# Performance work log

Measured on AMD Instinct MI355X. Metric: run time of the kernel, lower is better.

The kernel has to match this reference:

```python
import jax, jax.numpy as jnp
import numpy as np

N_NODES = 50000
N_EDGES = 800000
IN_DIM = 128
HIDDEN = 64
HEADS = 4
OUT_DIM = 64
NEG_SLOPE = 0.2


def setup_inputs() -> dict:
    key = jax.random.key(0)
    ks = jax.random.split(key, 16)
    def lin(k, fan_in, fan_out):
        return jax.random.normal(k, (fan_in, fan_out), dtype=jnp.float32) * (1.0 / np.sqrt(fan_in))
    def attn(k):
        return jax.random.normal(k, (HEADS, HIDDEN), dtype=jnp.float32) * 0.1
    inp = {
        "x": jax.random.normal(ks[0], (N_NODES, IN_DIM), dtype=jnp.float32),
        "src": jax.random.randint(ks[1], (N_EDGES,), 0, N_NODES, dtype=jnp.int32),
        "dst": jax.random.randint(ks[2], (N_EDGES,), 0, N_NODES, dtype=jnp.int32),
        # layer 0: in_dim -> heads*hidden
        "W0": lin(ks[3], IN_DIM, HEADS * HIDDEN),
        "al0": attn(ks[4]),
        "ar0": attn(ks[5]),
        # layer 1: heads*hidden -> heads*hidden
        "W1": lin(ks[6], HEADS * HIDDEN, HEADS * HIDDEN),
        "al1": attn(ks[7]),
        "ar1": attn(ks[8]),
        # final layer: heads*hidden -> heads*out_dim
        "W2": lin(ks[9], HEADS * HIDDEN, HEADS * OUT_DIM),
        "al2": jax.random.normal(ks[10], (HEADS, OUT_DIM), dtype=jnp.float32) * 0.1,
        "ar2": jax.random.normal(ks[11], (HEADS, OUT_DIM), dtype=jnp.float32) * 0.1,
        # output head: out_dim -> 1
        "Wout": lin(ks[12], OUT_DIM, 1),
        "bout": jnp.zeros((1,), dtype=jnp.float32),
    }
    return inp


def gat_layer(x, src, dst, W, al, ar):
    """DGL-style multi-head graph attention conv (edge gather/softmax/aggregate)."""
    N = x.shape[0]
    H, D = al.shape
    h = (x @ W).reshape(N, H, D)                      # [N,H,D]
    el = jnp.sum(h * al, axis=-1)                     # [N,H]
    er = jnp.sum(h * ar, axis=-1)                     # [N,H]
    e = jax.nn.leaky_relu(el[src] + er[dst], NEG_SLOPE)   # [E,H]
    # numerically-stable edge softmax segmented by destination node
    m = jax.ops.segment_max(e, dst, num_segments=N)   # [N,H]
    m = jnp.where(jnp.isfinite(m), m, 0.0)
    ex = jnp.exp(e - m[dst])                          # [E,H]
    denom = jax.ops.segment_sum(ex, dst, num_segments=N)  # [N,H]
    alpha = ex / (denom[dst] + 1e-9)                  # [E,H]
    msg = h[src] * alpha[..., None]                   # [E,H,D] (dominant traffic)
    out = jax.ops.segment_sum(msg, dst, num_segments=N)   # [N,H,D]
    return jax.nn.elu(out)


def reference(x, src, dst, W0, al0, ar0, W1, al1, ar1, W2, al2, ar2, Wout, bout):
    N = x.shape[0]
    # layer 0 (threshold layer also produces node index split index1/index0)
    h = gat_layer(x, src, dst, W0, al0, ar0)          # [N,H,HID]
    h = h.reshape(N, -1)                              # flatten(start=1,end=2)
    # middle layer
    h = gat_layer(h, src, dst, W1, al1, ar1)
    h = h.reshape(N, -1)
    # final layer + head-mean pool
    feats = gat_layer(h, src, dst, W2, al2, ar2)      # [N,H,OUT]
    feats = feats.mean(axis=1)                        # [N,OUT]
    out = jax.nn.relu(feats @ Wout + bout)            # [N,1]
    return out
```

## Files before the change

kernel.cpp:

```cpp
#include <hip/hip_runtime.h>
#include <hip/hip_fp16.h>
#include <math.h>

#define NN 50000
#define NE 800000
#define HEADS 4
#define HID 64
#define HD 256
#define NEG_SLOPE 0.2f
#define CSR_CAP 64

typedef __attribute__((ext_vector_type(8))) short short8;
typedef __attribute__((ext_vector_type(4))) float f32x4;
typedef __attribute__((ext_vector_type(2))) unsigned int uint2v;

__device__ __forceinline__ unsigned short f2bf(float f) {
    unsigned u = __float_as_uint(f);
    u += 0x7fff + ((u >> 16) & 1);
    return (unsigned short)(u >> 16);
}
__device__ __forceinline__ float bf2f(unsigned short b) {
    return __uint_as_float(((unsigned)b) << 16);
}

__device__ __forceinline__ float h2f_bits(unsigned short b) {
    __half_raw r; r.x = b;
    return __half2float(__half(r));
}
__device__ __forceinline__ unsigned short f2h_bits(float f) {
    __half_raw r(__float2half(f));
    return r.x;
}

__device__ __forceinline__ void wsplit_one(const float* W, unsigned short* Wf, int idx) {
    int lane = idx & 63;
    int tile = (idx >> 6) & 15;
    int kb   = idx >> 10;
    int col  = tile * 16 + (lane & 15);
    int krow = kb * 32 + (lane >> 4) * 8;
    unsigned short* p = Wf + ((size_t)(kb * 16 + tile) * 2 * 64 + lane) * 8;
#pragma unroll
    for (int j = 0; j < 8; j++) {
        float v = W[(size_t)(krow + j) * HD + col];
        unsigned short h = f2bf(v);
        unsigned short l = f2bf(v - bf2f(h));
        p[j] = h;
        p[512 + j] = l;
    }
}

__global__ __launch_bounds__(256) void prep_kernel(
    const float* __restrict__ W0, unsigned short* __restrict__ Wf0,
    const float* __restrict__ W1, unsigned short* __restrict__ Wf1,
    const float* __restrict__ W2, unsigned short* __restrict__ Wf2,
    int* __restrict__ cnt) {
    int b = (int)blockIdx.x;
    if (b < 80) {
        int idx = b * 256 + (int)threadIdx.x;
        const int n0 = 4 * 16 * 64;
        const int n1 = 8 * 16 * 64;
        if (idx < n0) wsplit_one(W0, Wf0, idx);
        else if (idx < n0 + n1) wsplit_one(W1, Wf1, idx - n0);
        else if (idx < n0 + 2 * n1) wsplit_one(W2, Wf2, idx - n0 - n1);
    } else {
        int base = (b - 80) * 1024 + (int)threadIdx.x;
#pragma unroll
        for (int j = 0; j < 4; j++) {
            int i = base + j * 256;
            if (i < NN) cnt[i] = 0;
        }
    }
}

__device__ __forceinline__ void gemm_epilogue(
    f32x4 (&acc)[4][4], int rowBase, int w, int mrow, int q,
    ushort* __restrict__ H, const float* __restrict__ al, const float* __restrict__ ar,
    float* __restrict__ el, float* __restrict__ er) {
    int n0 = w * 64;
    float alv[4], arv[4];
#pragma unroll
    for (int c = 0; c < 4; c++) {
        alv[c] = al[n0 + c * 16 + mrow];
        arv[c] = ar[n0 + c * 16 + mrow];
    }
#pragma unroll
    for (int r = 0; r < 4; r++) {
        float pl[4] = {0.f, 0.f, 0.f, 0.f};
        float pr[4] = {0.f, 0.f, 0.f, 0.f};
#pragma unroll
        for (int c = 0; c < 4; c++)
#pragma unroll
            for (int g = 0; g < 4; g++) {
                pl[g] += acc[r][c][g] * alv[c];
                pr[g] += acc[r][c][g] * arv[c];
            }
#pragma unroll
        for (int g = 0; g < 4; g++) {
#pragma unroll
            for (int off = 1; off < 16; off <<= 1) {
                pl[g] += __shfl_xor(pl[g], off);
                pr[g] += __shfl_xor(pr[g], off);
            }
        }
#pragma unroll
        for (int g = 0; g < 4; g++) {
            int row = rowBase + r * 16 + q * 4 + g;
            if (row < NN) {
#pragma unroll
                for (int c = 0; c < 4; c++)
                    H[(size_t)row * HD + n0 + c * 16 + mrow] = f2h_bits(acc[r][c][g]);
                if (mrow == 0) {
                    el[row * 4 + w] = pl[g];
                    er[row * 4 + w] = pr[g];
                }
            }
        }
    }
}

__device__ __forceinline__ void mfma_gemm_body_f32(
    int bid,
    const float* __restrict__ Xf,
    const unsigned short* __restrict__ Wf,
    ushort* __restrict__ H,
    const float* __restrict__ al, const float* __restrict__ ar,
    float* __restrict__ el, float* __restrict__ er,
    ushort* ldsA) {
    constexpr int K = 128;
    constexpr int KB = K / 32;
    int tid = (int)threadIdx.x;
    int w = tid >> 6;
    int lane = tid & 63;
    int rowBase = bid * 64;
    int mrow = lane & 15;
    int q = lane >> 4;

    f32x4 acc[4][4];
#pragma unroll
    for (int r = 0; r < 4; r++)
#pragma unroll
        for (int c = 0; c < 4; c++) {
            f32x4 z = {0.f, 0.f, 0.f, 0.f};
            acc[r][c] = z;
        }

    int srow = tid >> 2, qq = tid & 3;
    int grow = rowBase + srow;
    grow = grow < NN ? grow : NN - 1;
    int sr = srow >> 4, smrow = srow & 15;
    int flane = qq * 16 + smrow;
    ushort* sHi = &ldsA[((size_t)(sr * 2 + 0) * 64 + flane) * 8];

    float4 rf00, rf01, rf10, rf11;

    auto loadA0 = [&](int kb) {
        const float* xp = Xf + (size_t)grow * K + kb * 32 + qq * 8;
        rf00 = *(const float4*)xp;
        rf01 = *(const float4*)(xp + 4);
    };
    auto loadA1 = [&](int kb) {
        const float* xp = Xf + (size_t)grow * K + kb * 32 + qq * 8;
        rf10 = *(const float4*)xp;
        rf11 = *(const float4*)(xp + 4);
    };
    auto cvt8 = [&](float4 a, float4 b, short8& h8, short8& l8) {
        float vv[8] = {a.x, a.y, a.z, a.w, b.x, b.y, b.z, b.w};
#pragma unroll
        for (int j = 0; j < 8; j++) {
            unsigned short hh = f2bf(vv[j]);
            h8[j] = (short)hh;
            l8[j] = (short)f2bf(vv[j] - bf2f(hh));
        }
    };
    auto storeA0 = [&]() {
        short8 h8, l8;
        cvt8(rf00, rf01, h8, l8);
        *(short8*)sHi = h8;
        *(short8*)(sHi + 512) = l8;
    };
    auto storeA1 = [&]() {
        short8 h8, l8;
        cvt8(rf10, rf11, h8, l8);
        *(short8*)(sHi + 4096) = h8;
        *(short8*)(sHi + 4096 + 512) = l8;
    };

    auto compute = [&](int kb, int pofs) {
        short8 Wh[4], Wl_[4];
#pragma unroll
        for (int c = 0; c < 4; c++) {
            const unsigned short* wp =
                Wf + (((size_t)(kb * 16 + w * 4 + c) * 2) * 64 + lane) * 8;
            Wh[c]  = *(const short8*)wp;
            Wl_[c] = *(const short8*)(wp + 512);
        }
        short8 Ah[4], Al_[4];
#pragma unroll
        for (int r = 0; r < 4; r++) {
            Ah[r]  = *(const short8*)&ldsA[pofs + ((r * 2 + 0) * 64 + lane) * 8];
            Al_[r] = *(const short8*)&ldsA[pofs + ((r * 2 + 1) * 64 + lane) * 8];
        }
#pragma unroll
        for (int c = 0; c < 4; c++)
#pragma unroll
            for (int r = 0; r < 4; r++) {
                acc[r][c] = __builtin_amdgcn_mfma_f32_16x16x32_bf16(Ah[r],  Wh[c],  acc[r][c], 0, 0, 0);
                acc[r][c] = __builtin_amdgcn_mfma_f32_16x16x32_bf16(Ah[r],  Wl_[c], acc[r][c], 0, 0, 0);
                acc[r][c] = __builtin_amdgcn_mfma_f32_16x16x32_bf16(Al_[r], Wh[c],  acc[r][c], 0, 0, 0);
            }
    };

    loadA0(0);
    loadA1(1);
    for (int kb = 0; kb < KB; kb += 2) {
        __syncthreads();
        storeA0();
        storeA1();
        __syncthreads();
        if (kb + 2 < KB) {
            loadA0(kb + 2);
            loadA1(kb + 3);
        }
        compute(kb, 0);
        compute(kb + 1, 4096);
    }

    gemm_epilogue(acc, rowBase, w, mrow, q, H, al, ar, el, er);
}

__global__ __launch_bounds__(256, 3) void gemm0_scatter_kernel(
    const float* __restrict__ Xf, const unsigned short* __restrict__ Wf,
    ushort* __restrict__ H,
    const float* __restrict__ al, const float* __restrict__ ar,
    float* __restrict__ el, float* __restrict__ er,
    const int* __restrict__ src, const int* __restrict__ dst,
    int* __restrict__ cnt, int* __restrict__ csr_src) {
    __shared__ ushort ldsA[2 * 8 * 64 * 8];
    int b = (int)blockIdx.x;
    int g = b / 5, rem = b % 5;
    if (rem == 0) {
        mfma_gemm_body_f32(g, Xf, Wf, H, al, ar, el, er, ldsA);
    } else {
        int e = (g * 4 + (rem - 1)) * 256 + (int)threadIdx.x;
        if (e < NE) {
            int d = dst[e];
            int slot = atomicAdd(&cnt[d], 1);
            csr_src[(size_t)d * CSR_CAP + slot] = src[e];
        }
    }
}

__global__ __launch_bounds__(256, 2) void mfma_gemm_fullk_kernel(
    const ushort* __restrict__ Xh, const ushort* __restrict__ Xl,
    const unsigned short* __restrict__ Wf,
    ushort* __restrict__ H,
    const float* __restrict__ al, const float* __restrict__ ar,
    float* __restrict__ el, float* __restrict__ er) {
    constexpr int K = 256;
    constexpr int KB = K / 32;
    __shared__ ushort ldsA[KB * 4 * 2 * 64 * 8];
    int tid = (int)threadIdx.x;
    int w = tid >> 6;
    int lane = tid & 63;
    int rowBase = (int)blockIdx.x * 64;
    int mrow = lane & 15;
    int q = lane >> 4;

    int srow = tid >> 2, qq = tid & 3;
    int grow = rowBase + srow;
    grow = grow < NN ? grow : NN - 1;
    int sr = srow >> 4, smrow = srow & 15;
    int flane = qq * 16 + smrow;
    const ushort* xhp = Xh + (size_t)grow * K + qq * 8;
    const ushort* xlp = Xl + (size_t)grow * K + qq * 8;

    short8 sh[KB], sl[KB];
#pragma unroll
    for (int kb = 0; kb < KB; kb++) {
        sh[kb] = *(const short8*)(xhp + kb * 32);
        sl[kb] = *(const short8*)(xlp + kb * 32);
    }
#pragma unroll
    for (int kb = 0; kb < KB; kb++) {
        *(short8*)&ldsA[((size_t)(kb * 8 + sr * 2 + 0) * 64 + flane) * 8] = sh[kb];
        *(short8*)&ldsA[((size_t)(kb * 8 + sr * 2 + 1) * 64 + flane) * 8] = sl[kb];
    }
    __syncthreads();

    f32x4 acc[4][4];
#pragma unroll
    for (int r = 0; r < 4; r++)
#pragma unroll
        for (int c = 0; c < 4; c++) {
            f32x4 z = {0.f, 0.f, 0.f, 0.f};
            acc[r][c] = z;
        }

    for (int kb = 0; kb < KB; kb++) {
        const ushort* Abase = &ldsA[(size_t)kb * 8 * 512];
        short8 Wh[4], Wl_[4];
#pragma unroll
        for (int c = 0; c < 4; c++) {
            const unsigned short* wp =
                Wf + (((size_t)(kb * 16 + w * 4 + c) * 2) * 64 + lane) * 8;
            Wh[c]  = *(const short8*)wp;
            Wl_[c] = *(const short8*)(wp + 512);
        }
        short8 Ah[4], Al_[4];
#pragma unroll
        for (int r = 0; r < 4; r++) {
            Ah[r]  = *(const short8*)&Abase[((r * 2 + 0) * 64 + lane) * 8];
            Al_[r] = *(const short8*)&Abase[((r * 2 + 1) * 64 + lane) * 8];
        }
#pragma unroll
        for (int c = 0; c < 4; c++)
#pragma unroll
            for (int r = 0; r < 4; r++) {
                acc[r][c] = __builtin_amdgcn_mfma_f32_16x16x32_bf16(Ah[r],  Wh[c],  acc[r][c], 0, 0, 0);
                acc[r][c] = __builtin_amdgcn_mfma_f32_16x16x32_bf16(Ah[r],  Wl_[c], acc[r][c], 0, 0, 0);
                acc[r][c] = __builtin_amdgcn_mfma_f32_16x16x32_bf16(Al_[r], Wh[c],  acc[r][c], 0, 0, 0);
            }
    }

    gemm_epilogue(acc, rowBase, w, mrow, q, H, al, ar, el, er);
}

__device__ __forceinline__ float lrelu(float x) { return fmaxf(x, NEG_SLOPE * x); }

__device__ __forceinline__ float4 us4tof4(ushort4 u) {
    float4 f;
    f.x = h2f_bits(u.x); f.y = h2f_bits(u.y);
    f.z = h2f_bits(u.z); f.w = h2f_bits(u.w);
    return f;
}

template <int FINAL>
__global__ __launch_bounds__(256) void gat_node_kernel(
    const ushort* __restrict__ H, const float* __restrict__ el, const float* __restrict__ er,
    const int* __restrict__ cnt, const int* __restrict__ csr_src,
    ushort* __restrict__ out_hi, ushort* __restrict__ out_lo,
    const float* __restrict__ Wout, const float* __restrict__ bout,
    float* __restrict__ final_out) {
    int wave = threadIdx.x >> 6, lane = threadIdx.x & 63;
    int v = blockIdx.x * 4 + wave;
    if (v >= NN) return;
    int beg = v * CSR_CAP;
    int end = beg + cnt[v];

    int hh = lane >> 4;
    float er_h = er[v * 4 + hh];
    const float* elh = el + hh;
    unsigned lane4 = (unsigned)(lane * 4);

    float ss0 = 0.f, ss1 = 0.f, ss2 = 0.f, ss3 = 0.f;
    float4 a0 = make_float4(0.f, 0.f, 0.f, 0.f);
    float4 a1 = make_float4(0.f, 0.f, 0.f, 0.f);
    float4 a2 = make_float4(0.f, 0.f, 0.f, 0.f);
    float4 a3 = make_float4(0.f, 0.f, 0.f, 0.f);
    {
        int i = beg;
        for (; i + 4 <= end; i += 4) {
            unsigned s0 = (unsigned)csr_src[i];
            unsigned s1 = (unsigned)csr_src[i + 1];
            unsigned s2 = (unsigned)csr_src[i + 2];
            unsigned s3 = (unsigned)csr_src[i + 3];
            ushort4 q0 = *(const ushort4*)(H + ((s0 << 8) + lane4));
            ushort4 q1 = *(const ushort4*)(H + ((s1 << 8) + lane4));
            ushort4 q2 = *(const ushort4*)(H + ((s2 << 8) + lane4));
            ushort4 q3 = *(const ushort4*)(H + ((s3 << 8) + lane4));
            float w0 = __expf(lrelu(elh[s0 * 4u] + er_h));
            float w1 = __expf(lrelu(elh[s1 * 4u] + er_h));
            float w2 = __expf(lrelu(elh[s2 * 4u] + er_h));
            float w3 = __expf(lrelu(elh[s3 * 4u] + er_h));
            float4 h0 = us4tof4(q0);
            float4 h1 = us4tof4(q1);
            float4 h2 = us4tof4(q2);
            float4 h3 = us4tof4(q3);
            ss0 += w0; ss1 += w1; ss2 += w2; ss3 += w3;
            a0.x += w0 * h0.x; a0.y += w0 * h0.y; a0.z += w0 * h0.z; a0.w += w0 * h0.w;
            a1.x += w1 * h1.x; a1.y += w1 * h1.y; a1.z += w1 * h1.z; a1.w += w1 * h1.w;
            a2.x += w2 * h2.x; a2.y += w2 * h2.y; a2.z += w2 * h2.z; a2.w += w2 * h2.w;
            a3.x += w3 * h3.x; a3.y += w3 * h3.y; a3.z += w3 * h3.z; a3.w += w3 * h3.w;
        }
        for (; i < end; i++) {
            unsigned s0 = (unsigned)csr_src[i];
            ushort4 q0 = *(const ushort4*)(H + ((s0 << 8) + lane4));
            float w0 = __expf(lrelu(elh[s0 * 4u] + er_h));
            float4 h0 = us4tof4(q0);
            ss0 += w0;
            a0.x += w0 * h0.x; a0.y += w0 * h0.y; a0.z += w0 * h0.z; a0.w += w0 * h0.w;
        }
    }
    float ssum = (ss0 + ss1) + (ss2 + ss3);
    float4 acc;
    acc.x = (a0.x + a1.x) + (a2.x + a3.x);
    acc.y = (a0.y + a1.y) + (a2.y + a3.y);
    acc.z = (a0.z + a1.z) + (a2.z + a3.z);
    acc.w = (a0.w + a1.w) + (a2.w + a3.w);

    float inv = 1.0f / (ssum + 1e-9f);
    acc.x *= inv; acc.y *= inv; acc.z *= inv; acc.w *= inv;

    acc.x = acc.x > 0.f ? acc.x : expm1f(acc.x);
    acc.y = acc.y > 0.f ? acc.y : expm1f(acc.y);
    acc.z = acc.z > 0.f ? acc.z : expm1f(acc.z);
    acc.w = acc.w > 0.f ? acc.w : expm1f(acc.w);

    if (!FINAL) {
        ushort4 hv, lv;
        hv.x = f2bf(acc.x); lv.x = f2bf(acc.x - bf2f(hv.x));
        hv.y = f2bf(acc.y); lv.y = f2bf(acc.y - bf2f(hv.y));
        hv.z = f2bf(acc.z); lv.z = f2bf(acc.z - bf2f(hv.z));
        hv.w = f2bf(acc.w); lv.w = f2bf(acc.w - bf2f(hv.w));
        uint2v ph = { (unsigned)hv.x | ((unsigned)hv.y << 16),
                      (unsigned)hv.z | ((unsigned)hv.w << 16) };
        uint2v pl = { (unsigned)lv.x | ((unsigned)lv.y << 16),
                      (unsigned)lv.z | ((unsigned)lv.w << 16) };
        __builtin_nontemporal_store(ph, (uint2v*)(out_hi + (size_t)v * HD + lane * 4));
        __builtin_nontemporal_store(pl, (uint2v*)(out_lo + (size_t)v * HD + lane * 4));
    } else {
        acc.x += __shfl_xor(acc.x, 16); acc.x += __shfl_xor(acc.x, 32);
        acc.y += __shfl_xor(acc.y, 16); acc.y += __shfl_xor(acc.y, 32);
        acc.z += __shfl_xor(acc.z, 16); acc.z += __shfl_xor(acc.z, 32);
        acc.w += __shfl_xor(acc.w, 16); acc.w += __shfl_xor(acc.w, 32);
        float4 w4 = *(const float4*)&Wout[(lane & 15) * 4];
        float p = 0.25f * (acc.x * w4.x + acc.y * w4.y + acc.z * w4.z + acc.w * w4.w);
        p += __shfl_xor(p, 1);
        p += __shfl_xor(p, 2);
        p += __shfl_xor(p, 4);
        p += __shfl_xor(p, 8);
        if (lane == 0) final_out[v] = fmaxf(p + bout[0], 0.f);
    }
}

extern "C" void kernel_launch(void* const* d_in, const int* in_sizes, int n_in,
                              void* d_out, int out_size, void* d_ws, size_t ws_size,
                              hipStream_t stream) {
    const float* x    = (const float*)d_in[0];
    const int*   src  = (const int*)d_in[1];
    const int*   dst  = (const int*)d_in[2];
    const float* W0   = (const float*)d_in[3];
    const float* al0  = (const float*)d_in[4];
    const float* ar0  = (const float*)d_in[5];
    const float* W1   = (const float*)d_in[6];
    const float* al1  = (const float*)d_in[7];
    const float* ar1  = (const float*)d_in[8];
    const float* W2   = (const float*)d_in[9];
    const float* al2  = (const float*)d_in[10];
    const float* ar2  = (const float*)d_in[11];
    const float* Wout = (const float*)d_in[12];
    const float* bout = (const float*)d_in[13];
    float* outp = (float*)d_out;

    char* ws = (char*)d_ws;
    size_t off = 0;
    auto carve = [&](size_t n) -> char* {
        char* p = ws + off;
        off += (n + 255) & ~(size_t)255;
        return p;
    };
    ushort* h_buf  = (ushort*)carve((size_t)NN * HD * 2);
    ushort* xh     = (ushort*)carve((size_t)NN * HD * 2);
    ushort* xl     = (ushort*)carve((size_t)NN * HD * 2);
    float*  el     = (float*)carve((size_t)NN * HEADS * 4);
    float*  er     = (float*)carve((size_t)NN * HEADS * 4);
    int*    cnt    = (int*)carve((size_t)NN * 4);
    int*    csr_src= (int*)carve((size_t)NN * CSR_CAP * 4);
    unsigned short* Wf0 = (unsigned short*)carve((size_t)4 * 16 * 64 * 16 * 2);
    unsigned short* Wf1 = (unsigned short*)carve((size_t)8 * 16 * 64 * 16 * 2);
    unsigned short* Wf2 = (unsigned short*)carve((size_t)8 * 16 * 64 * 16 * 2);

    const int gGemm = (NN + 63) / 64;
    const int gNode = (NN + 3) / 4;
    const int nZeroBlk = (NN + 1023) / 1024;

    prep_kernel<<<80 + nZeroBlk, 256, 0, stream>>>(W0, Wf0, W1, Wf1, W2, Wf2, cnt);
    gemm0_scatter_kernel<<<gGemm * 5, 256, 0, stream>>>(
        x, Wf0, h_buf, al0, ar0, el, er, src, dst, cnt, csr_src);
    gat_node_kernel<0><<<gNode, 256, 0, stream>>>(h_buf, el, er, cnt, csr_src,
                                                  xh, xl, nullptr, nullptr, nullptr);
    mfma_gemm_fullk_kernel<<<gGemm, 256, 0, stream>>>(xh, xl, Wf1,
                                                      h_buf, al1, ar1, el, er);
    gat_node_kernel<0><<<gNode, 256, 0, stream>>>(h_buf, el, er, cnt, csr_src,
                                                  xh, xl, nullptr, nullptr, nullptr);
    mfma_gemm_fullk_kernel<<<gGemm, 256, 0, stream>>>(xh, xl, Wf2,
                                                      h_buf, al2, ar2, el, er);
    gat_node_kernel<1><<<gNode, 256, 0, stream>>>(h_buf, el, er, cnt, csr_src,
                                                  nullptr, nullptr, Wout, bout, outp);
}
```

Measured before the change: 404.3 us.

## Fuse GAT aggregation into following GEMM via LDS, drop split-bf16 intermediate buffers

Merges the per-node attention aggregation of layers 0 and 1 into the next layer's MFMA GEMM kernel. Each 512-thread block aggregates 64 nodes and writes the bf16 hi/lo split straight into LDS, so the xh/xl global round-trip and two launches go away. H and el/er are ping-ponged between two buffers, and the edge loop is unrolled by 8. The trade-off is that the gather phase now runs at 8 nodes per wave sequentially with GEMM waves idle, which may reduce latency hiding compared to the separate node kernel.

```diff
diff --git a/kernel.cpp b/kernel.cpp
--- a/kernel.cpp
+++ b/kernel.cpp
@@ -12,7 +12,6 @@
 
 typedef __attribute__((ext_vector_type(8))) short short8;
 typedef __attribute__((ext_vector_type(4))) float f32x4;
-typedef __attribute__((ext_vector_type(2))) unsigned int uint2v;
 
 __device__ __forceinline__ unsigned short f2bf(float f) {
     unsigned u = __float_as_uint(f);
@@ -30,6 +29,15 @@
 __device__ __forceinline__ unsigned short f2h_bits(float f) {
     __half_raw r(__float2half(f));
     return r.x;
+}
+
+__device__ __forceinline__ float lrelu(float x) { return fmaxf(x, NEG_SLOPE * x); }
+
+__device__ __forceinline__ float4 us4tof4(ushort4 u) {
+    float4 f;
+    f.x = h2f_bits(u.x); f.y = h2f_bits(u.y);
+    f.z = h2f_bits(u.z); f.w = h2f_bits(u.w);
+    return f;
 }
 
 __device__ __forceinline__ void wsplit_one(const float* W, unsigned short* Wf, int idx) {
@@ -250,95 +258,223 @@
     }
 }
 
-__global__ __launch_bounds__(256, 2) void mfma_gemm_fullk_kernel(
-    const ushort* __restrict__ Xh, const ushort* __restrict__ Xl,
+__global__ __launch_bounds__(512, 4) void fused_gat_gemm_kernel(
+    const ushort* __restrict__ H_in, const float* __restrict__ el_in,
+    const float* __restrict__ er_in,
+    const int* __restrict__ cnt, const int* __restrict__ csr_src,
     const unsigned short* __restrict__ Wf,
-    ushort* __restrict__ H,
+    ushort* __restrict__ H_out,
     const float* __restrict__ al, const float* __restrict__ ar,
-    float* __restrict__ el, float* __restrict__ er) {
-    constexpr int K = 256;
-    constexpr int KB = K / 32;
+    float* __restrict__ el_out, float* __restrict__ er_out) {
+    constexpr int KB = 8;
     __shared__ ushort ldsA[KB * 4 * 2 * 64 * 8];
     int tid = (int)threadIdx.x;
-    int w = tid >> 6;
+    int wv = tid >> 6;
     int lane = tid & 63;
     int rowBase = (int)blockIdx.x * 64;
+
+    {
+        int hh = lane >> 4;
+        unsigned lane4 = (unsigned)(lane * 4);
+        const float* elh = el_in + hh;
+        int c0 = lane * 4;
+        int kb_w = c0 >> 5;
+        int qq_w = (c0 >> 3) & 3;
+        int j0_w = c0 & 7;
+#pragma unroll 1
+        for (int n = 0; n < 8; n++) {
+            int srow = wv * 8 + n;
+            int v = rowBase + srow;
+            float4 acc = make_float4(0.f, 0.f, 0.f, 0.f);
+            if (v < NN) {
+                int beg = v * CSR_CAP;
+                int end = beg + cnt[v];
+                float er_h = er_in[v * 4 + hh];
+                float ss0 = 0.f, ss1 = 0.f, ss2 = 0.f, ss3 = 0.f;
+                float4 a0 = make_float4(0.f, 0.f, 0.f, 0.f);
+                float4 a1 = make_float4(0.f, 0.f, 0.f, 0.f);
+                float4 a2 = make_float4(0.f, 0.f, 0.f, 0.f);
+                float4 a3 = make_float4(0.f, 0.f, 0.f, 0.f);
+                int i = beg;
+                for (; i + 8 <= end; i += 8) {
+                    unsigned s0 = (unsigned)csr_src[i];
+                    unsigned s1 = (unsigned)csr_src[i + 1];
+                    unsigned s2 = (unsigned)csr_src[i + 2];
+                    unsigned s3 = (unsigned)csr_src[i + 3];
+                    unsigned s4 = (unsigned)csr_src[i + 4];
+                    unsigned s5 = (unsigned)csr_src[i + 5];
+                    unsigned s6 = (unsigned)csr_src[i + 6];
+                    unsigned s7 = (unsigned)csr_src[i + 7];
+                    ushort4 q0 = *(const ushort4*)(H_in + ((s0 << 8) + lane4));
+                    ushort4 q1 = *(const ushort4*)(H_in + ((s1 << 8) + lane4));
+                    ushort4 q2 = *(const ushort4*)(H_in + ((s2 << 8) + lane4));
+                    ushort4 q3 = *(const ushort4*)(H_in + ((s3 << 8) + lane4));
+                    ushort4 q4 = *(const ushort4*)(H_in + ((s4 << 8) + lane4));
+                    ushort4 q5 = *(const ushort4*)(H_in + ((s5 << 8) + lane4));
+                    ushort4 q6 = *(const ushort4*)(H_in + ((s6 << 8) + lane4));
+                    ushort4 q7 = *(const ushort4*)(H_in + ((s7 << 8) + lane4));
+                    float w0 = __expf(lrelu(elh[s0 * 4u] + er_h));
+                    float w1 = __expf(lrelu(elh[s1 * 4u] + er_h));
+                    float w2 = __expf(lrelu(elh[s2 * 4u] + er_h));
+                    float w3 = __expf(lrelu(elh[s3 * 4u] + er_h));
+                    float w4 = __expf(lrelu(elh[s4 * 4u] + er_h));
+                    float w5 = __expf(lrelu(elh[s5 * 4u] + er_h));
+                    float w6 = __expf(lrelu(elh[s6 * 4u] + er_h));
+                    float w7 = __expf(lrelu(elh[s7 * 4u] + er_h));
+                    float4 h0 = us4tof4(q0), h1 = us4tof4(q1);
+                    float4 h2 = us4tof4(q2), h3 = us4tof4(q3);
+                    float4 h4 = us4tof4(q4), h5 = us4tof4(q5);
+                    float4 h6 = us4tof4(q6), h7 = us4tof4(q7);
+                    ss0 += w0 + w4; ss1 += w1 + w5; ss2 += w2 + w6; ss3 += w3 + w7;
+                    a0.x += w0 * h0.x + w4 * h4.x; a0.y += w0 * h0.y + w4 * h4.y;
+                    a0.z += w0 * h0.z + w4 * h4.z; a0.w += w0 * h0.w + w4 * h4.w;
+                    a1.x += w1 * h1.x + w5 * h5.x; a1.y += w1 * h1.y + w5 * h5.y;
+                    a1.z += w1 * h1.z + w5 * h5.z; a1.w += w1 * h1.w + w5 * h5.w;
+                    a2.x += w2 * h2.x + w6 * h6.x; a2.y += w2 * h2.y + w6 * h6.y;
+                    a2.z += w2 * h2.z + w6 * h6.z; a2.w += w2 * h2.w + w6 * h6.w;
+                    a3.x += w3 * h3.x + w7 * h7.x; a3.y += w3 * h3.y + w7 * h7.y;
+                    a3.z += w3 * h3.z + w7 * h7.z; a3.w += w3 * h3.w + w7 * h7.w;
+                }
+                for (; i + 4 <= end; i += 4) {
+                    unsigned s0 = (unsigned)csr_src[i];
+                    unsigned s1 = (unsigned)csr_src[i + 1];
+                    unsigned s2 = (unsigned)csr_src[i + 2];
+                    unsigned s3 = (unsigned)csr_src[i + 3];
+                    ushort4 q0 = *(const ushort4*)(H_in + ((s0 << 8) + lane4));
+                    ushort4 q1 = *(const ushort4*)(H_in + ((s1 << 8) + lane4));
+                    ushort4 q2 = *(const ushort4*)(H_in + ((s2 << 8) + lane4));
+                    ushort4 q3 = *(const ushort4*)(H_in + ((s3 << 8) + lane4));
+                    float w0 = __expf(lrelu(elh[s0 * 4u] + er_h));
+                    float w1 = __expf(lrelu(elh[s1 * 4u] + er_h));
+                    float w2 = __expf(lrelu(elh[s2 * 4u] + er_h));
+                    float w3 = __expf(lrelu(elh[s3 * 4u] + er_h));
+                    float4 h0 = us4tof4(q0), h1 = us4tof4(q1);
+                    float4 h2 = us4tof4(q2), h3 = us4tof4(q3);
+                    ss0 += w0; ss1 += w1; ss2 += w2; ss3 += w3;
+                    a0.x += w0 * h0.x; a0.y += w0 * h0.y; a0.z += w0 * h0.z; a0.w += w0 * h0.w;
+                    a1.x += w1 * h1.x; a1.y += w1 * h1.y; a1.z += w1 * h1.z; a1.w += w1 * h1.w;
+                    a2.x += w2 * h2.x; a2.y += w2 * h2.y; a2.z += w2 * h2.z; a2.w += w2 * h2.w;
+                    a3.x += w3 * h3.x; a3.y += w3 * h3.y; a3.z += w3 * h3.z; a3.w += w3 * h3.w;
+                }
+                for (; i < end; i++) {
+                    unsigned s0 = (unsigned)csr_src[i];
+                    ushort4 q0 = *(const ushort4*)(H_in + ((s0 << 8) + lane4));
+                    float w0 = __expf(lrelu(elh[s0 * 4u] + er_h));
+                    float4 h0 = us4tof4(q0);
+                    ss0 += w0;
+                    a0.x += w0 * h0.x; a0.y += w0 * h0.y; a0.z += w0 * h0.z; a0.w += w0 * h0.w;
+                }
+                float ssum = (ss0 + ss1) + (ss2 + ss3);
+                float inv = 1.0f / (ssum + 1e-9f);
+                acc.x = ((a0.x + a1.x) + (a2.x + a3.x)) * inv;
+                acc.y = ((a0.y + a1.y) + (a2.y + a3.y)) * inv;
+                acc.z = ((a0.z + a1.z) + (a2.z + a3.z)) * inv;
+                acc.w = ((a0.w + a1.w) + (a2.w + a3.w)) * inv;
+                acc.x = acc.x > 0.f ? acc.x : expm1f(acc.x);
+                acc.y = acc.y > 0.f ? acc.y : expm1f(acc.y);
+                acc.z = acc.z > 0.f ? acc.z : expm1f(acc.z);
+                acc.w = acc.w > 0.f ? acc.w : expm1f(acc.w);
+            }
+            ushort4 hv, lv;
+            hv.x = f2bf(acc.x); lv.x = f2bf(acc.x - bf2f(hv.x));
+            hv.y = f2bf(acc.y); lv.y = f2bf(acc.y - bf2f(hv.y));
+            hv.z = f2bf(acc.z); lv.z = f2bf(acc.z - bf2f(hv.z));
+            hv.w = f2bf(acc.w); lv.w = f2bf(acc.w - bf2f(hv.w));
+            int sr = srow >> 4, smrow = srow & 15;
+            size_t idx = ((size_t)((kb_w * 8 + sr * 2 + 0) * 64) + qq_w * 16 + smrow) * 8 + j0_w;
+            *(ushort4*)&ldsA[idx] = hv;
+            *(ushort4*)&ldsA[idx + 512] = lv;
+        }
+    }
+    __syncthreads();
+
+    int hw = wv & 3;
+    int rh = wv >> 2;
     int mrow = lane & 15;
     int q = lane >> 4;
 
-    int srow = tid >> 2, qq = tid & 3;
-    int grow = rowBase + srow;
-    grow = grow < NN ? grow : NN - 1;
-    int sr = srow >> 4, smrow = srow & 15;
-    int flane = qq * 16 + smrow;
-    const ushort* xhp = Xh + (size_t)grow * K + qq * 8;
-    const ushort* xlp = Xl + (size_t)grow * K + qq * 8;
-
-    short8 sh[KB], sl[KB];
-#pragma unroll
-    for (int kb = 0; kb < KB; kb++) {
-        sh[kb] = *(const short8*)(xhp + kb * 32);
-        sl[kb] = *(const short8*)(xlp + kb * 32);
-    }
-#pragma unroll
-    for (int kb = 0; kb < KB; kb++) {
-        *(short8*)&ldsA[((size_t)(kb * 8 + sr * 2 + 0) * 64 + flane) * 8] = sh[kb];
-        *(short8*)&ldsA[((size_t)(kb * 8 + sr * 2 + 1) * 64 + flane) * 8] = sl[kb];
-    }
-    __syncthreads();
-
-    f32x4 acc[4][4];
-#pragma unroll
-    for (int r = 0; r < 4; r++)
+    f32x4 acc2[2][4];
+#pragma unroll
+    for (int r = 0; r < 2; r++)
 #pragma unroll
         for (int c = 0; c < 4; c++) {
             f32x4 z = {0.f, 0.f, 0.f, 0.f};
-            acc[r][c] = z;
+            acc2[r][c] = z;
         }
 
     for (int kb = 0; kb < KB; kb++) {
-        const ushort* Abase = &ldsA[(size_t)kb * 8 * 512];
         short8 Wh[4], Wl_[4];
 #pragma unroll
         for (int c = 0; c < 4; c++) {
             const unsigned short* wp =
-                Wf + (((size_t)(kb * 16 + w * 4 + c) * 2) * 64 + lane) * 8;
+                Wf + (((size_t)(kb * 16 + hw * 4 + c) * 2) * 64 + lane) * 8;
             Wh[c]  = *(const short8*)wp;
             Wl_[c] = *(const short8*)(wp + 512);
         }
-        short8 Ah[4], Al_[4];
-#pragma unroll
-        for (int r = 0; r < 4; r++) {
-            Ah[r]  = *(const short8*)&Abase[((r * 2 + 0) * 64 + lane) * 8];
-            Al_[r] = *(const short8*)&Abase[((r * 2 + 1) * 64 + lane) * 8];
+        short8 Ah[2], Al_[2];
+#pragma unroll
+        for (int r = 0; r < 2; r++) {
+            int rp = rh * 2 + r;
+            Ah[r]  = *(const short8*)&ldsA[((size_t)((kb * 8 + rp * 2 + 0) * 64) + lane) * 8];
+            Al_[r] = *(const short8*)&ldsA[((size_t)((kb * 8 + rp * 2 + 1) * 64) + lane) * 8];
         }
 #pragma unroll
         for (int c = 0; c < 4; c++)
 #pragma unroll
-            for (int r = 0; r < 4; r++) {
-                acc[r][c] = __builtin_amdgcn_mfma_f32_16x16x32_bf16(Ah[r],  Wh[c],  acc[r][c], 0, 0, 0);
-                acc[r][c] = __builtin_amdgcn_mfma_f32_16x16x32_bf16(Ah[r],  Wl_[c], acc[r][c], 0, 0, 0);
-                acc[r][c] = __builtin_amdgcn_mfma_f32_16x16x32_bf16(Al_[r], Wh[c],  acc[r][c], 0, 0, 0);
-            }
-    }
-
-    gemm_epilogue(acc, rowBase, w, mrow, q, H, al, ar, el, er);
-}
-
-__device__ __forceinline__ float lrelu(float x) { return fmaxf(x, NEG_SLOPE * x); }
-
-__device__ __forceinline__ float4 us4tof4(ushort4 u) {
-    float4 f;
-    f.x = h2f_bits(u.x); f.y = h2f_bits(u.y);
-    f.z = h2f_bits(u.z); f.w = h2f_bits(u.w);
-    return f;
-}
-
-template <int FINAL>
-__global__ __launch_bounds__(256) void gat_node_kernel(
+            for (int r = 0; r < 2; r++) {
+                acc2[r][c] = __builtin_amdgcn_mfma_f32_16x16x32_bf16(Ah[r],  Wh[c],  acc2[r][c], 0, 0, 0);
+                acc2[r][c] = __builtin_amdgcn_mfma_f32_16x16x32_bf16(Ah[r],  Wl_[c], acc2[r][c], 0, 0, 0);
+                acc2[r][c] = __builtin_amdgcn_mfma_f32_16x16x32_bf16(Al_[r], Wh[c],  acc2[r][c], 0, 0, 0);
+            }
+    }
+
+    {
+        int n0 = hw * 64;
+        float alv[4], arv[4];
+#pragma unroll
+        for (int c = 0; c < 4; c++) {
+            alv[c] = al[n0 + c * 16 + mrow];
+            arv[c] = ar[n0 + c * 16 + mrow];
+        }
+#pragma unroll
+        for (int r = 0; r < 2; r++) {
+            float pl[4] = {0.f, 0.f, 0.f, 0.f};
+            float pr[4] = {0.f, 0.f, 0.f, 0.f};
+#pragma unroll
+            for (int c = 0; c < 4; c++)
+#pragma unroll
+                for (int g = 0; g < 4; g++) {
+                    pl[g] += acc2[r][c][g] * alv[c];
+                    pr[g] += acc2[r][c][g] * arv[c];
+                }
+#pragma unroll
+            for (int g = 0; g < 4; g++) {
+#pragma unroll
+                for (int off = 1; off < 16; off <<= 1) {
+                    pl[g] += __shfl_xor(pl[g], off);
+                    pr[g] += __shfl_xor(pr[g], off);
+                }
+            }
+#pragma unroll
+            for (int g = 0; g < 4; g++) {
+                int row = rowBase + rh * 32 + r * 16 + q * 4 + g;
+                if (row < NN) {
+#pragma unroll
+                    for (int c = 0; c < 4; c++)
+                        H_out[(size_t)row * HD + n0 + c * 16 + mrow] = f2h_bits(acc2[r][c][g]);
+                    if (mrow == 0) {
+                        el_out[row * 4 + hw] = pl[g];
+                        er_out[row * 4 + hw] = pr[g];
+                    }
+                }
+            }
+        }
+    }
+}
+
+__global__ __launch_bounds__(256) void gat_final_kernel(
     const ushort* __restrict__ H, const float* __restrict__ el, const float* __restrict__ er,
     const int* __restrict__ cnt, const int* __restrict__ csr_src,
-    ushort* __restrict__ out_hi, ushort* __restrict__ out_lo,
     const float* __restrict__ Wout, const float* __restrict__ bout,
     float* __restrict__ final_out) {
     int wave = threadIdx.x >> 6, lane = threadIdx.x & 63;
@@ -372,10 +508,8 @@
             float w1 = __expf(lrelu(elh[s1 * 4u] + er_h));
             float w2 = __expf(lrelu(elh[s2 * 4u] + er_h));
             float w3 = __expf(lrelu(elh[s3 * 4u] + er_h));
-            float4 h0 = us4tof4(q0);
-            float4 h1 = us4tof4(q1);
-            float4 h2 = us4tof4(q2);
-            float4 h3 = us4tof4(q3);
+            float4 h0 = us4tof4(q0), h1 = us4tof4(q1);
+            float4 h2 = us4tof4(q2), h3 = us4tof4(q3);
             ss0 += w0; ss1 += w1; ss2 += w2; ss3 += w3;
             a0.x += w0 * h0.x; a0.y += w0 * h0.y; a0.z += w0 * h0.z; a0.w += w0 * h0.w;
             a1.x += w1 * h1.x; a1.y += w1 * h1.y; a1.z += w1 * h1.z; a1.w += w1 * h1.w;
@@ -406,31 +540,17 @@
     acc.z = acc.z > 0.f ? acc.z : expm1f(acc.z);
     acc.w = acc.w > 0.f ? acc.w : expm1f(acc.w);
 
-    if (!FINAL) {
-        ushort4 hv, lv;
-        hv.x = f2bf(acc.x); lv.x = f2bf(acc.x - bf2f(hv.x));
-        hv.y = f2bf(acc.y); lv.y = f2bf(acc.y - bf2f(hv.y));
-        hv.z = f2bf(acc.z); lv.z = f2bf(acc.z - bf2f(hv.z));
-        hv.w = f2bf(acc.w); lv.w = f2bf(acc.w - bf2f(hv.w));
-        uint2v ph = { (unsigned)hv.x | ((unsigned)hv.y << 16),
-                      (unsigned)hv.z | ((unsigned)hv.w << 16) };
-        uint2v pl = { (unsigned)lv.x | ((unsigned)lv.y << 16),
-                      (unsigned)lv.z | ((unsigned)lv.w << 16) };
-        __builtin_nontemporal_store(ph, (uint2v*)(out_hi + (size_t)v * HD + lane * 4));
-        __builtin_nontemporal_store(pl, (uint2v*)(out_lo + (size_t)v * HD + lane * 4));
-    } else {
-        acc.x += __shfl_xor(acc.x, 16); acc.x += __shfl_xor(acc.x, 32);
-        acc.y += __shfl_xor(acc.y, 16); acc.y += __shfl_xor(acc.y, 32);
-        acc.z += __shfl_xor(acc.z, 16); acc.z += __shfl_xor(acc.z, 32);
-        acc.w += __shfl_xor(acc.w, 16); acc.w += __shfl_xor(acc.w, 32);
-        float4 w4 = *(const float4*)&Wout[(lane & 15) * 4];
-        float p = 0.25f * (acc.x * w4.x + acc.y * w4.y + acc.z * w4.z + acc.w * w4.w);
-        p += __shfl_xor(p, 1);
-        p += __shfl_xor(p, 2);
-        p += __shfl_xor(p, 4);
-        p += __shfl_xor(p, 8);
-        if (lane == 0) final_out[v] = fmaxf(p + bout[0], 0.f);
-    }
+    acc.x += __shfl_xor(acc.x, 16); acc.x += __shfl_xor(acc.x, 32);
+    acc.y += __shfl_xor(acc.y, 16); acc.y += __shfl_xor(acc.y, 32);
+    acc.z += __shfl_xor(acc.z, 16); acc.z += __shfl_xor(acc.z, 32);
+    acc.w += __shfl_xor(acc.w, 16); acc.w += __shfl_xor(acc.w, 32);
+    float4 w4 = *(const float4*)&Wout[(lane & 15) * 4];
+    float p = 0.25f * (acc.x * w4.x + acc.y * w4.y + acc.z * w4.z + acc.w * w4.w);
+    p += __shfl_xor(p, 1);
+    p += __shfl_xor(p, 2);
+    p += __shfl_xor(p, 4);
+    p += __shfl_xor(p, 8);
+    if (lane == 0) final_out[v] = fmaxf(p + bout[0], 0.f);
 }
 
 extern "C" void kernel_launch(void* const* d_in, const int* in_sizes, int n_in,
@@ -459,13 +579,14 @@
         off += (n + 255) & ~(size_t)255;
         return p;
     };
-    ushort* h_buf  = (ushort*)carve((size_t)NN * HD * 2);
-    ushort* xh     = (ushort*)carve((size_t)NN * HD * 2);
-    ushort* xl     = (ushort*)carve((size_t)NN * HD * 2);
-    float*  el     = (float*)carve((size_t)NN * HEADS * 4);
-    float*  er     = (float*)carve((size_t)NN * HEADS * 4);
-    int*    cnt    = (int*)carve((size_t)NN * 4);
-    int*    csr_src= (int*)carve((size_t)NN * CSR_CAP * 4);
+    ushort* hA    = (ushort*)carve((size_t)NN * HD * 2);
+    ushort* hB    = (ushort*)carve((size_t)NN * HD * 2);
+    float*  elA   = (float*)carve((size_t)NN * HEADS * 4);
+    float*  erA   = (float*)carve((size_t)NN * HEADS * 4);
+    float*  elB   = (float*)carve((size_t)NN * HEADS * 4);
+    float*  erB   = (float*)carve((size_t)NN * HEADS * 4);
+    int*    cnt   = (int*)carve((size_t)NN * 4);
+    int*    csr_src = (int*)carve((size_t)NN * CSR_CAP * 4);
     unsigned short* Wf0 = (unsigned short*)carve((size_t)4 * 16 * 64 * 16 * 2);
     unsigned short* Wf1 = (unsigned short*)carve((size_t)8 * 16 * 64 * 16 * 2);
     unsigned short* Wf2 = (unsigned short*)carve((size_t)8 * 16 * 64 * 16 * 2);
@@ -476,15 +597,11 @@
 
     prep_kernel<<<80 + nZeroBlk, 256, 0, stream>>>(W0, Wf0, W1, Wf1, W2, Wf2, cnt);
     gemm0_scatter_kernel<<<gGemm * 5, 256, 0, stream>>>(
-        x, Wf0, h_buf, al0, ar0, el, er, src, dst, cnt, csr_src);
-    gat_node_kernel<0><<<gNode, 256, 0, stream>>>(h_buf, el, er, cnt, csr_src,
-                                                  xh, xl, nullptr, nullptr, nullptr);
-    mfma_gemm_fullk_kernel<<<gGemm, 256, 0, stream>>>(xh, xl, Wf1,
-                                                      h_buf, al1, ar1, el, er);
-    gat_node_kernel<0><<<gNode, 256, 0, stream>>>(h_buf, el, er, cnt, csr_src,
-                                                  xh, xl, nullptr, nullptr, nullptr);
-    mfma_gemm_fullk_kernel<<<gGemm, 256, 0, stream>>>(xh, xl, Wf2,
-                                                      h_buf, al2, ar2, el, er);
-    gat_node_kernel<1><<<gNode, 256, 0, stream>>>(h_buf, el, er, cnt, csr_src,
-                                                  nullptr, nullptr, Wout, bout, outp);
-}
+        x, Wf0, hA, al0, ar0, elA, erA, src, dst, cnt, csr_src);
+    fused_gat_gemm_kernel<<<gGemm, 512, 0, stream>>>(
+        hA, elA, erA, cnt, csr_src, Wf1, hB, al1, ar1, elB, erB);
+    fused_gat_gemm_kernel<<<gGemm, 512, 0, stream>>>(
+        hB, elB, erB, cnt, csr_src, Wf2, hA, al2, ar2, elA, erA);
+    gat_final_kernel<<<gNode, 256, 0, stream>>>(hA, elA, erA, cnt, csr_src,
+                                                Wout, bout, outp);
+}
```

After: 417.5 us. +3.3%, slower.
